# Optimization experiments

Measured on AMD Instinct MI355X. Metric: run time of the kernel, lower is better.

Reference implementation:

```python
import jax, jax.numpy as jnp
import numpy as np

EPS = 1e-5


def conv1x1(x, w, b):
    # x: [b,c,h,w], w: [o,c], b: [o] -> [b,o,h,w]  (1x1 conv == channel matmul)
    return jnp.einsum('bchw,oc->bohw', x, w) + b[None, :, None, None]


def nor_mean_std(x):
    # instance norm over spatial dims (torch calc_mean_std uses unbiased var)
    mean = jnp.mean(x, axis=(2, 3), keepdims=True)
    var = jnp.var(x, axis=(2, 3), keepdims=True, ddof=1)
    return (x - mean) / jnp.sqrt(var + EPS)


def nor_mean(x):
    mean = jnp.mean(x, axis=(2, 3), keepdims=True)
    return x - mean, mean


def net(x, w1, b1, w2, b2):
    return conv1x1(jax.nn.relu(conv1x1(x, w1, b1)), w2, b2)


def setup_inputs() -> dict:
    key = jax.random.key(0)
    ks = jax.random.split(key, 8)
    B, C, H, W = 8, 256, 128, 128
    return {
        'content': jax.random.normal(ks[0], (B, C, H, W), jnp.float32),
        'style': jax.random.normal(ks[1], (B, C, H, W), jnp.float32),
        'w1': jax.random.normal(ks[2], (128, 256), jnp.float32) * 0.05,
        'b1': jax.random.normal(ks[3], (128,), jnp.float32) * 0.05,
        'w2': jax.random.normal(ks[4], (32, 128), jnp.float32) * 0.05,
        'b2': jax.random.normal(ks[5], (32,), jnp.float32) * 0.05,
        'wu': jax.random.normal(ks[6], (256, 32), jnp.float32) * 0.05,
        'bu': jax.random.normal(ks[7], (256,), jnp.float32) * 0.05,
    }


def reference(content, style, w1, b1, w2, b2, wu, bu):
    cF_nor = nor_mean_std(content)
    sF_nor, smean = nor_mean(style)
    cF = net(cF_nor, w1, b1, w2, b2)          # [b,32,h,w]
    sF = net(sF_nor, w1, b1, w2, b2)          # [b,32,h,w]
    b, c, h, w = cF.shape
    hw = h * w
    sf = sF.reshape(b, c, hw)
    # channel covariance: [b,32,32]
    s_cov = jnp.einsum('bcn,bdn->bcd', sf, sf) / hw
    s_cov = jax.nn.softmax(s_cov, axis=-1) * (c ** -0.5)
    gF = jnp.einsum('bcd,bdn->bcn', s_cov, cF.reshape(b, c, hw)).reshape(b, c, h, w)
    gF = conv1x1(gF, wu, bu)                  # [b,256,h,w]
    return gF + smean + content
```

## Files before the change

### kernel.cpp

```cpp
#include <hip/hip_runtime.h>

#define HW 16384
#define C_IN 256
#define C_MID 128
#define C_OUT 32
#define EPSF 1e-5f

typedef __bf16 bf16x8 __attribute__((ext_vector_type(8)));
typedef __bf16 bf16x4 __attribute__((ext_vector_type(4)));
typedef float f32x4 __attribute__((ext_vector_type(4)));

__device__ __forceinline__ bf16x4 cvt4(f32x4 v) {
    bf16x4 r;
    r[0] = (__bf16)v[0]; r[1] = (__bf16)v[1];
    r[2] = (__bf16)v[2]; r[3] = (__bf16)v[3];
    return r;
}

__global__ __launch_bounds__(512) void k_stats10(const float* __restrict__ content,
                                                 const float* __restrict__ style,
                                                 float* __restrict__ cmean,
                                                 float* __restrict__ crstd,
                                                 float* __restrict__ smean,
                                                 __bf16* __restrict__ cbf,
                                                 __bf16* __restrict__ sbf) {
    const int bc = blockIdx.x;
    const int t = threadIdx.x;
    const f32x4* cp = (const f32x4*)(content + (size_t)bc * HW);
    const f32x4* sp = (const f32x4*)(style + (size_t)bc * HW);
    const int phase = (bc * 257) & 4095;

    int idx[8];
    #pragma unroll
    for (int i = 0; i < 8; ++i) idx[i] = (phase + t + i * 512) & 4095;

    f32x4 c[8], s[8];
    #pragma unroll
    for (int i = 0; i < 8; ++i) c[i] = __builtin_nontemporal_load(cp + idx[i]);
    #pragma unroll
    for (int i = 0; i < 8; ++i) s[i] = __builtin_nontemporal_load(sp + idx[i]);
    asm volatile("" ::
        "v"(c[0]), "v"(c[1]), "v"(c[2]), "v"(c[3]), "v"(c[4]), "v"(c[5]), "v"(c[6]), "v"(c[7]),
        "v"(s[0]), "v"(s[1]), "v"(s[2]), "v"(s[3]), "v"(s[4]), "v"(s[5]), "v"(s[6]), "v"(s[7]));

    {
        bf16x4* cb = (bf16x4*)(cbf + (size_t)bc * HW);
        bf16x4* sb = (bf16x4*)(sbf + (size_t)bc * HW);
        #pragma unroll
        for (int i = 0; i < 8; ++i) {
            cb[idx[i]] = cvt4(c[i]);
            sb[idx[i]] = cvt4(s[i]);
        }
    }

    float cs, cq, ss;
    {
        f32x4 a01 = c[0] + c[1], a23 = c[2] + c[3], a45 = c[4] + c[5], a67 = c[6] + c[7];
        f32x4 a = (a01 + a23) + (a45 + a67);
        cs = (a[0] + a[1]) + (a[2] + a[3]);
        f32x4 q01 = c[0]*c[0] + c[1]*c[1], q23 = c[2]*c[2] + c[3]*c[3];
        f32x4 q45 = c[4]*c[4] + c[5]*c[5], q67 = c[6]*c[6] + c[7]*c[7];
        f32x4 q = (q01 + q23) + (q45 + q67);
        cq = (q[0] + q[1]) + (q[2] + q[3]);
        f32x4 b01 = s[0] + s[1], b23 = s[2] + s[3], b45 = s[4] + s[5], b67 = s[6] + s[7];
        f32x4 bsum = (b01 + b23) + (b45 + b67);
        ss = (bsum[0] + bsum[1]) + (bsum[2] + bsum[3]);
    }

    #pragma unroll
    for (int d = 32; d > 0; d >>= 1) {
        cs += __shfl_xor(cs, d, 64);
        cq += __shfl_xor(cq, d, 64);
        ss += __shfl_xor(ss, d, 64);
    }
    __shared__ float rs[8], rq[8], rss[8];
    const int wv = t >> 6;
    if ((t & 63) == 0) { rs[wv] = cs; rq[wv] = cq; rss[wv] = ss; }
    __syncthreads();
    if (t == 0) {
        float S = 0.f, Q = 0.f, SS = 0.f;
        #pragma unroll
        for (int i = 0; i < 8; ++i) { S += rs[i]; Q += rq[i]; SS += rss[i]; }
        float n = (float)HW;
        float var = (Q - S * S / n) / (n - 1.f);
        cmean[bc] = S / n;
        crstd[bc] = 1.f / sqrtf(var + EPSF);
        smean[bc] = SS / n;
    }
}

__global__ __launch_bounds__(256) void k_wprep2(const float* __restrict__ w1,
                                                const float* __restrict__ b1,
                                                const float* __restrict__ w2,
                                                const float* __restrict__ cmean,
                                                const float* __restrict__ crstd,
                                                const float* __restrict__ smean,
                                                __bf16* __restrict__ W1c,
                                                float* __restrict__ bias1c,
                                                __bf16* __restrict__ W1s,
                                                float* __restrict__ bias1s,
                                                __bf16* __restrict__ W2b) {
    int o = blockIdx.x, b = blockIdx.y, t = threadIdx.x;
    float w = w1[o * 256 + t];
    float r = crstd[b * 256 + t];
    float wc = w * r;
    W1c[((size_t)(b * 128 + o)) * 256 + t] = (__bf16)wc;
    if (b == 0) {
        W1s[o * 256 + t] = (__bf16)w;
        if (t < 32) W2b[o * 32 + t] = (__bf16)w2[o * 32 + t];
    }
    float pc = wc * cmean[b * 256 + t];
    float ps = w * smean[b * 256 + t];
    __shared__ float rA[256], rB[256];
    rA[t] = pc; rB[t] = ps;
    __syncthreads();
    for (int off = 128; off > 0; off >>= 1) {
        if (t < off) { rA[t] += rA[t + off]; rB[t] += rB[t + off]; }
        __syncthreads();
    }
    if (t == 0) {
        bias1c[b * 128 + o] = b1[o] - rA[0];
        bias1s[b * 128 + o] = b1[o] - rB[0];
    }
}

template <int MODE>
__global__ __launch_bounds__(256) void k_net_bf(const __bf16* __restrict__ x,
                                                const __bf16* __restrict__ W1,
                                                const float* __restrict__ bias1,
                                                const __bf16* __restrict__ W2,
                                                const float* __restrict__ b2,
                                                float* __restrict__ outF,
                                                float* __restrict__ partial,
                                                int w1_per_batch) {
    __shared__ __bf16 Xl[64 * 256];
    __shared__ __bf16 Tl[64 * 128];
    const int tid = threadIdx.x;
    const int l = tid & 63, wv = tid >> 6;
    const int lr = l & 15, g = l >> 4;
    const int sw = (lr & 7) << 4;
    const int p0 = blockIdx.x * 64;
    const int b = blockIdx.y;
    const __bf16* xb = x + (size_t)b * C_IN * HW;

    {
        const int p = wv * 16 + lr;
        const __bf16* xp = xb + p0 + p;
        char* row = (char*)&Xl[p * 256];
        #pragma unroll 4
        for (int cc = 0; cc < 16; ++cc) {
            const int c = cc * 16 + g * 4;
            bf16x4 v;
            v[0] = xp[(size_t)(c + 0) * HW];
            v[1] = xp[(size_t)(c + 1) * HW];
            v[2] = xp[(size_t)(c + 2) * HW];
            v[3] = xp[(size_t)(c + 3) * HW];
            *(bf16x4*)(row + ((c * 2) ^ sw)) = v;
        }
    }
    __syncthreads();

    const f32x4 zero4 = {0.f, 0.f, 0.f, 0.f};
    f32x4 acc[2][4];
    #pragma unroll
    for (int mt = 0; mt < 2; ++mt)
        #pragma unroll
        for (int nt = 0; nt < 4; ++nt) acc[mt][nt] = zero4;

    const __bf16* W1b = W1 + (w1_per_batch ? ((size_t)b << 15) : 0);
    const __bf16* wrow0 = W1b + (size_t)(wv * 32 + lr) * 256 + g * 8;
    const __bf16* wrow1 = wrow0 + 16 * 256;

    #pragma unroll
    for (int kt = 0; kt < 8; ++kt) {
        bf16x8 a0 = *(const bf16x8*)(wrow0 + kt * 32);
        bf16x8 a1 = *(const bf16x8*)(wrow1 + kt * 32);
        #pragma unroll
        for (int nt = 0; nt < 4; ++nt) {
            const char* xrow = (const char*)&Xl[(nt * 16 + lr) * 256];
            bf16x8 bfr = *(const bf16x8*)(xrow + (((kt * 32 + g * 8) * 2) ^ sw));
            acc[0][nt] = __builtin_amdgcn_mfma_f32_16x16x32_bf16(a0, bfr, acc[0][nt], 0, 0, 0);
            acc[1][nt] = __builtin_amdgcn_mfma_f32_16x16x32_bf16(a1, bfr, acc[1][nt], 0, 0, 0);
        }
    }

    float4 bia[2];
    bia[0] = *(const float4*)&bias1[b * 128 + wv * 32 + g * 4];
    bia[1] = *(const float4*)&bias1[b * 128 + wv * 32 + 16 + g * 4];
    __syncthreads();
    #pragma unroll
    for (int mt = 0; mt < 2; ++mt) {
        #pragma unroll
        for (int nt = 0; nt < 4; ++nt) {
            const int p = nt * 16 + lr;
            char* trow = (char*)&Tl[p * 128];
            const int ob = (wv * 32 + mt * 16 + g * 4) * 2;
            bf16x4 tv;
            tv[0] = (__bf16)fmaxf(acc[mt][nt][0] + bia[mt].x, 0.f);
            tv[1] = (__bf16)fmaxf(acc[mt][nt][1] + bia[mt].y, 0.f);
            tv[2] = (__bf16)fmaxf(acc[mt][nt][2] + bia[mt].z, 0.f);
            tv[3] = (__bf16)fmaxf(acc[mt][nt][3] + bia[mt].w, 0.f);
            *(bf16x4*)(trow + (ob ^ sw)) = tv;
        }
    }
    __syncthreads();

    f32x4 acc2[2];
    acc2[0] = zero4; acc2[1] = zero4;
    const int p = wv * 16 + lr;
    const char* trow = (const char*)&Tl[p * 128];
    const __bf16* w2r0 = W2 + (size_t)lr * 128 + g * 8;
    const __bf16* w2r1 = w2r0 + 16 * 128;
    #pragma unroll
    for (int kt = 0; kt < 4; ++kt) {
        bf16x8 bfr = *(const bf16x8*)(trow + (((kt * 32 + g * 8) * 2) ^ sw));
        bf16x8 a0 = *(const bf16x8*)(w2r0 + kt * 32);
        bf16x8 a1 = *(const bf16x8*)(w2r1 + kt * 32);
        acc2[0] = __builtin_amdgcn_mfma_f32_16x16x32_bf16(a0, bfr, acc2[0], 0, 0, 0);
        acc2[1] = __builtin_amdgcn_mfma_f32_16x16x32_bf16(a1, bfr, acc2[1], 0, 0, 0);
    }
    float4 bb0 = *(const float4*)&b2[g * 4];
    float4 bb1 = *(const float4*)&b2[16 + g * 4];
    const int o0 = g * 4;

    if constexpr (MODE == 0) {
        float* ob = outF + (size_t)b * C_OUT * HW + p0 + p;
        ob[(size_t)(o0 + 0) * HW] = acc2[0][0] + bb0.x;
        ob[(size_t)(o0 + 1) * HW] = acc2[0][1] + bb0.y;
        ob[(size_t)(o0 + 2) * HW] = acc2[0][2] + bb0.z;
        ob[(size_t)(o0 + 3) * HW] = acc2[0][3] + bb0.w;
        ob[(size_t)(16 + o0 + 0) * HW] = acc2[1][0] + bb1.x;
        ob[(size_t)(16 + o0 + 1) * HW] = acc2[1][1] + bb1.y;
        ob[(size_t)(16 + o0 + 2) * HW] = acc2[1][2] + bb1.z;
        ob[(size_t)(16 + o0 + 3) * HW] = acc2[1][3] + bb1.w;
    } else {
        float* gt = (float*)Xl;
        gt[(o0 + 0) * 65 + p] = acc2[0][0] + bb0.x;
        gt[(o0 + 1) * 65 + p] = acc2[0][1] + bb0.y;
        gt[(o0 + 2) * 65 + p] = acc2[0][2] + bb0.z;
        gt[(o0 + 3) * 65 + p] = acc2[0][3] + bb0.w;
        gt[(16 + o0 + 0) * 65 + p] = acc2[1][0] + bb1.x;
        gt[(16 + o0 + 1) * 65 + p] = acc2[1][1] + bb1.y;
        gt[(16 + o0 + 2) * 65 + p] = acc2[1][2] + bb1.z;
        gt[(16 + o0 + 3) * 65 + p] = acc2[1][3] + bb1.w;
        __syncthreads();
        const int gi = tid >> 3, jb = (tid & 7) * 4;
        float g4[4] = {0.f, 0.f, 0.f, 0.f};
        #pragma unroll 8
        for (int n = 0; n < 64; ++n) {
            float si = gt[gi * 65 + n];
            #pragma unroll
            for (int q = 0; q < 4; ++q)
                g4[q] = fmaf(si, gt[(jb + q) * 65 + n], g4[q]);
        }
        float* dst = partial + ((size_t)(b * 256 + blockIdx.x)) * 1024 + tid * 4;
        #pragma unroll
        for (int q = 0; q < 4; ++q) dst[q] = g4[q];
    }
}

__global__ __launch_bounds__(1024) void k_softmax2(const float* __restrict__ partial,
                                                   float* __restrict__ scov) {
    int b = blockIdx.x;
    int j = threadIdx.x, i = threadIdx.y;
    const float* base = partial + (size_t)b * 256 * 1024 + i * 32 + j;
    float v0 = 0.f, v1 = 0.f, v2 = 0.f, v3 = 0.f;
    #pragma unroll 4
    for (int s = 0; s < 256; s += 4) {
        v0 += base[(s + 0) * 1024];
        v1 += base[(s + 1) * 1024];
        v2 += base[(s + 2) * 1024];
        v3 += base[(s + 3) * 1024];
    }
    float v = ((v0 + v1) + (v2 + v3)) * (1.f / (float)HW);
    float m = v;
    #pragma unroll
    for (int d = 16; d > 0; d >>= 1) m = fmaxf(m, __shfl_xor(m, d, 32));
    float e = expf(v - m);
    float sum = e;
    #pragma unroll
    for (int d = 16; d > 0; d >>= 1) sum += __shfl_xor(sum, d, 32);
    scov[(size_t)b * 1024 + i * 32 + j] = e / sum * 0.17677669529663687f;
}

__global__ __launch_bounds__(256) void k_final3(const float* __restrict__ cF,
                                                const float* __restrict__ scov,
                                                const float* __restrict__ wu,
                                                const float* __restrict__ bu,
                                                const float* __restrict__ smean,
                                                const __bf16* __restrict__ cbf,
                                                float* __restrict__ out) {
    __shared__ float sCov[1024];
    __shared__ float sC[32 * 64];
    __shared__ float sG[32 * 64];
    int t = threadIdx.x;
    int p0 = blockIdx.x * 64;
    int b = blockIdx.y;
    #pragma unroll
    for (int q = 0; q < 4; ++q) sCov[t + 256 * q] = scov[(size_t)b * 1024 + t + 256 * q];
    {
        int p = t & 63, rb = t >> 6;
        #pragma unroll
        for (int pass = 0; pass < 8; ++pass) {
            int r = pass * 4 + rb;
            sC[r * 64 + p] = cF[(size_t)b * C_OUT * HW + (size_t)r * HW + p0 + p];
        }
    }
    __syncthreads();
    {
        int gp = t & 63, gib = (t >> 6) * 8;
        #pragma unroll
        for (int rr = 0; rr < 8; ++rr) {
            int gi = gib + rr;
            float a = 0.f;
            #pragma unroll
            for (int k = 0; k < 32; ++k)
                a = fmaf(sCov[gi * 32 + k], sC[k * 64 + gp], a);
            sG[gi * 64 + gp] = a;
        }
    }
    __syncthreads();
    int tx = t & 7, ty = t >> 3;
    const float* wurow = wu + (size_t)(ty * 8) * 32;
    float acc[8][8];
    #pragma unroll
    for (int i = 0; i < 8; ++i)
        #pragma unroll
        for (int j = 0; j < 8; ++j) acc[i][j] = 0.f;
    #pragma unroll 4
    for (int k = 0; k < 32; ++k) {
        float a[8];
        #pragma unroll
        for (int i = 0; i < 8; ++i) a[i] = wurow[i * 32 + k];
        float4 b4a = *(const float4*)&sG[k * 64 + tx * 8];
        float4 b4b = *(const float4*)&sG[k * 64 + tx * 8 + 4];
        float bb[8] = {b4a.x, b4a.y, b4a.z, b4a.w, b4b.x, b4b.y, b4b.z, b4b.w};
        #pragma unroll
        for (int i = 0; i < 8; ++i)
            #pragma unroll
            for (int j = 0; j < 8; ++j)
                acc[i][j] = fmaf(a[i], bb[j], acc[i][j]);
    }
    #pragma unroll
    for (int i = 0; i < 8; ++i) {
        int o = ty * 8 + i;
        float add = bu[o] + smean[b * 256 + o];
        const __bf16* csrc = cbf + (size_t)b * C_IN * HW + (size_t)o * HW + p0 + tx * 8;
        float* dst = out + (size_t)b * C_IN * HW + (size_t)o * HW + p0 + tx * 8;
        bf16x8 cvv = *(const bf16x8*)csrc;
        f32x4 r0 = {acc[i][0] + add + (float)cvv[0], acc[i][1] + add + (float)cvv[1],
                    acc[i][2] + add + (float)cvv[2], acc[i][3] + add + (float)cvv[3]};
        f32x4 r1 = {acc[i][4] + add + (float)cvv[4], acc[i][5] + add + (float)cvv[5],
                    acc[i][6] + add + (float)cvv[6], acc[i][7] + add + (float)cvv[7]};
        __builtin_nontemporal_store(r0, (f32x4*)dst);
        __builtin_nontemporal_store(r1, (f32x4*)(dst + 4));
    }
}

extern "C" void kernel_launch(void* const* d_in, const int* in_sizes, int n_in,
                              void* d_out, int out_size, void* d_ws, size_t ws_size,
                              hipStream_t stream) {
    const float* content = (const float*)d_in[0];
    const float* style   = (const float*)d_in[1];
    const float* w1      = (const float*)d_in[2];
    const float* b1      = (const float*)d_in[3];
    const float* w2      = (const float*)d_in[4];
    const float* b2      = (const float*)d_in[5];
    const float* wu      = (const float*)d_in[6];
    const float* bu      = (const float*)d_in[7];
    float* out = (float*)d_out;
    float* ws  = (float*)d_ws;

    float* cmean   = ws;
    float* crstd   = ws + 2048;
    float* smean   = ws + 4096;
    float* scov    = ws + 6144;
    float* bias1c  = ws + 14336;
    float* bias1s  = ws + 15360;
    __bf16* W2b    = (__bf16*)(ws + 16384);
    __bf16* W1s    = (__bf16*)(ws + 18432);
    __bf16* W1c    = (__bf16*)(ws + 34816);
    float* partial = ws + 165888;
    float* cF      = ws + 2263040;
    __bf16* cbf    = (__bf16*)(ws + 6457344);
    __bf16* sbf    = (__bf16*)(ws + 23234560);

    k_stats10<<<dim3(2048), 512, 0, stream>>>(content, style, cmean, crstd, smean, cbf, sbf);
    k_wprep2<<<dim3(128, 8), 256, 0, stream>>>(w1, b1, w2, cmean, crstd, smean,
                                               W1c, bias1c, W1s, bias1s, W2b);
    k_net_bf<0><<<dim3(256, 8), 256, 0, stream>>>(cbf, W1c, bias1c, W2b, b2, cF, nullptr, 1);
    k_net_bf<1><<<dim3(256, 8), 256, 0, stream>>>(sbf, W1s, bias1s, W2b, b2, nullptr, partial, 0);
    k_softmax2<<<dim3(8), dim3(32, 32), 0, stream>>>(partial, scov);
    k_final3<<<dim3(256, 8), 256, 0, stream>>>(cF, scov, wu, bu, smean, cbf, out);
}
```

Measured before the change: 245.4 us.

## Fuse content net into final kernel, drop cF round trip and reuse staged content

Moves the content-branch net (two 1x1 convs on bf16 content) into the final kernel. cF is no longer written to and read back from global memory. The residual content values are now read from the bf16 tile already staged in shared memory instead of being loaded again from global. This removes one launch and the cF traffic, at the cost of more shared memory per block (the Xl, Tl, sCov and sG buffers together) and lower occupancy in the fused kernel.

```diff
diff --git a/kernel.cpp b/kernel.cpp
--- a/kernel.cpp
+++ b/kernel.cpp
@@ -124,15 +124,12 @@
     }
 }
 
-template <int MODE>
-__global__ __launch_bounds__(256) void k_net_bf(const __bf16* __restrict__ x,
-                                                const __bf16* __restrict__ W1,
-                                                const float* __restrict__ bias1,
-                                                const __bf16* __restrict__ W2,
-                                                const float* __restrict__ b2,
-                                                float* __restrict__ outF,
-                                                float* __restrict__ partial,
-                                                int w1_per_batch) {
+__global__ __launch_bounds__(256) void k_net_s(const __bf16* __restrict__ x,
+                                               const __bf16* __restrict__ W1,
+                                               const float* __restrict__ bias1,
+                                               const __bf16* __restrict__ W2,
+                                               const float* __restrict__ b2,
+                                               float* __restrict__ partial) {
     __shared__ __bf16 Xl[64 * 256];
     __shared__ __bf16 Tl[64 * 128];
     const int tid = threadIdx.x;
@@ -167,8 +164,7 @@
         #pragma unroll
         for (int nt = 0; nt < 4; ++nt) acc[mt][nt] = zero4;
 
-    const __bf16* W1b = W1 + (w1_per_batch ? ((size_t)b << 15) : 0);
-    const __bf16* wrow0 = W1b + (size_t)(wv * 32 + lr) * 256 + g * 8;
+    const __bf16* wrow0 = W1 + (size_t)(wv * 32 + lr) * 256 + g * 8;
     const __bf16* wrow1 = wrow0 + 16 * 256;
 
     #pragma unroll
@@ -223,40 +219,28 @@
     float4 bb1 = *(const float4*)&b2[16 + g * 4];
     const int o0 = g * 4;
 
-    if constexpr (MODE == 0) {
-        float* ob = outF + (size_t)b * C_OUT * HW + p0 + p;
-        ob[(size_t)(o0 + 0) * HW] = acc2[0][0] + bb0.x;
-        ob[(size_t)(o0 + 1) * HW] = acc2[0][1] + bb0.y;
-        ob[(size_t)(o0 + 2) * HW] = acc2[0][2] + bb0.z;
-        ob[(size_t)(o0 + 3) * HW] = acc2[0][3] + bb0.w;
-        ob[(size_t)(16 + o0 + 0) * HW] = acc2[1][0] + bb1.x;
-        ob[(size_t)(16 + o0 + 1) * HW] = acc2[1][1] + bb1.y;
-        ob[(size_t)(16 + o0 + 2) * HW] = acc2[1][2] + bb1.z;
-        ob[(size_t)(16 + o0 + 3) * HW] = acc2[1][3] + bb1.w;
-    } else {
-        float* gt = (float*)Xl;
-        gt[(o0 + 0) * 65 + p] = acc2[0][0] + bb0.x;
-        gt[(o0 + 1) * 65 + p] = acc2[0][1] + bb0.y;
-        gt[(o0 + 2) * 65 + p] = acc2[0][2] + bb0.z;
-        gt[(o0 + 3) * 65 + p] = acc2[0][3] + bb0.w;
-        gt[(16 + o0 + 0) * 65 + p] = acc2[1][0] + bb1.x;
-        gt[(16 + o0 + 1) * 65 + p] = acc2[1][1] + bb1.y;
-        gt[(16 + o0 + 2) * 65 + p] = acc2[1][2] + bb1.z;
-        gt[(16 + o0 + 3) * 65 + p] = acc2[1][3] + bb1.w;
-        __syncthreads();
-        const int gi = tid >> 3, jb = (tid & 7) * 4;
-        float g4[4] = {0.f, 0.f, 0.f, 0.f};
-        #pragma unroll 8
-        for (int n = 0; n < 64; ++n) {
-            float si = gt[gi * 65 + n];
-            #pragma unroll
-            for (int q = 0; q < 4; ++q)
-                g4[q] = fmaf(si, gt[(jb + q) * 65 + n], g4[q]);
-        }
-        float* dst = partial + ((size_t)(b * 256 + blockIdx.x)) * 1024 + tid * 4;
-        #pragma unroll
-        for (int q = 0; q < 4; ++q) dst[q] = g4[q];
-    }
+    float* gt = (float*)Xl;
+    gt[(o0 + 0) * 65 + p] = acc2[0][0] + bb0.x;
+    gt[(o0 + 1) * 65 + p] = acc2[0][1] + bb0.y;
+    gt[(o0 + 2) * 65 + p] = acc2[0][2] + bb0.z;
+    gt[(o0 + 3) * 65 + p] = acc2[0][3] + bb0.w;
+    gt[(16 + o0 + 0) * 65 + p] = acc2[1][0] + bb1.x;
+    gt[(16 + o0 + 1) * 65 + p] = acc2[1][1] + bb1.y;
+    gt[(16 + o0 + 2) * 65 + p] = acc2[1][2] + bb1.z;
+    gt[(16 + o0 + 3) * 65 + p] = acc2[1][3] + bb1.w;
+    __syncthreads();
+    const int gi = tid >> 3, jb = (tid & 7) * 4;
+    float g4[4] = {0.f, 0.f, 0.f, 0.f};
+    #pragma unroll 8
+    for (int n = 0; n < 64; ++n) {
+        float si = gt[gi * 65 + n];
+        #pragma unroll
+        for (int q = 0; q < 4; ++q)
+            g4[q] = fmaf(si, gt[(jb + q) * 65 + n], g4[q]);
+    }
+    float* dst = partial + ((size_t)(b * 256 + blockIdx.x)) * 1024 + tid * 4;
+    #pragma unroll
+    for (int q = 0; q < 4; ++q) dst[q] = g4[q];
 }
 
 __global__ __launch_bounds__(1024) void k_softmax2(const float* __restrict__ partial,
@@ -283,32 +267,126 @@
     scov[(size_t)b * 1024 + i * 32 + j] = e / sum * 0.17677669529663687f;
 }
 
-__global__ __launch_bounds__(256) void k_final3(const float* __restrict__ cF,
-                                                const float* __restrict__ scov,
-                                                const float* __restrict__ wu,
-                                                const float* __restrict__ bu,
-                                                const float* __restrict__ smean,
-                                                const __bf16* __restrict__ cbf,
-                                                float* __restrict__ out) {
+__global__ __launch_bounds__(256) void k_netc_final(const __bf16* __restrict__ x,
+                                                    const __bf16* __restrict__ W1,
+                                                    const float* __restrict__ bias1,
+                                                    const __bf16* __restrict__ W2,
+                                                    const float* __restrict__ b2,
+                                                    const float* __restrict__ scov,
+                                                    const float* __restrict__ wu,
+                                                    const float* __restrict__ bu,
+                                                    const float* __restrict__ smean,
+                                                    float* __restrict__ out) {
+    __shared__ __bf16 Xl[64 * 256];
+    __shared__ __bf16 Tl[64 * 128];
     __shared__ float sCov[1024];
-    __shared__ float sC[32 * 64];
     __shared__ float sG[32 * 64];
-    int t = threadIdx.x;
-    int p0 = blockIdx.x * 64;
-    int b = blockIdx.y;
-    #pragma unroll
-    for (int q = 0; q < 4; ++q) sCov[t + 256 * q] = scov[(size_t)b * 1024 + t + 256 * q];
-    {
-        int p = t & 63, rb = t >> 6;
-        #pragma unroll
-        for (int pass = 0; pass < 8; ++pass) {
-            int r = pass * 4 + rb;
-            sC[r * 64 + p] = cF[(size_t)b * C_OUT * HW + (size_t)r * HW + p0 + p];
-        }
-    }
-    __syncthreads();
-    {
-        int gp = t & 63, gib = (t >> 6) * 8;
+    const int tid = threadIdx.x;
+    const int l = tid & 63, wv = tid >> 6;
+    const int lr = l & 15, g = l >> 4;
+    const int sw = (lr & 7) << 4;
+    const int p0 = blockIdx.x * 64;
+    const int b = blockIdx.y;
+    const __bf16* xb = x + (size_t)b * C_IN * HW;
+
+    #pragma unroll
+    for (int q = 0; q < 4; ++q)
+        sCov[tid + 256 * q] = scov[(size_t)b * 1024 + tid + 256 * q];
+    {
+        const int p = wv * 16 + lr;
+        const __bf16* xp = xb + p0 + p;
+        char* row = (char*)&Xl[p * 256];
+        #pragma unroll 4
+        for (int cc = 0; cc < 16; ++cc) {
+            const int c = cc * 16 + g * 4;
+            bf16x4 v;
+            v[0] = xp[(size_t)(c + 0) * HW];
+            v[1] = xp[(size_t)(c + 1) * HW];
+            v[2] = xp[(size_t)(c + 2) * HW];
+            v[3] = xp[(size_t)(c + 3) * HW];
+            *(bf16x4*)(row + ((c * 2) ^ sw)) = v;
+        }
+    }
+    __syncthreads();
+
+    const f32x4 zero4 = {0.f, 0.f, 0.f, 0.f};
+    f32x4 acc1[2][4];
+    #pragma unroll
+    for (int mt = 0; mt < 2; ++mt)
+        #pragma unroll
+        for (int nt = 0; nt < 4; ++nt) acc1[mt][nt] = zero4;
+
+    const __bf16* W1b = W1 + ((size_t)b << 15);
+    const __bf16* wrow0 = W1b + (size_t)(wv * 32 + lr) * 256 + g * 8;
+    const __bf16* wrow1 = wrow0 + 16 * 256;
+
+    #pragma unroll
+    for (int kt = 0; kt < 8; ++kt) {
+        bf16x8 a0 = *(const bf16x8*)(wrow0 + kt * 32);
+        bf16x8 a1 = *(const bf16x8*)(wrow1 + kt * 32);
+        #pragma unroll
+        for (int nt = 0; nt < 4; ++nt) {
+            const char* xrow = (const char*)&Xl[(nt * 16 + lr) * 256];
+            bf16x8 bfr = *(const bf16x8*)(xrow + (((kt * 32 + g * 8) * 2) ^ sw));
+            acc1[0][nt] = __builtin_amdgcn_mfma_f32_16x16x32_bf16(a0, bfr, acc1[0][nt], 0, 0, 0);
+            acc1[1][nt] = __builtin_amdgcn_mfma_f32_16x16x32_bf16(a1, bfr, acc1[1][nt], 0, 0, 0);
+        }
+    }
+
+    float4 bia[2];
+    bia[0] = *(const float4*)&bias1[b * 128 + wv * 32 + g * 4];
+    bia[1] = *(const float4*)&bias1[b * 128 + wv * 32 + 16 + g * 4];
+    #pragma unroll
+    for (int mt = 0; mt < 2; ++mt) {
+        #pragma unroll
+        for (int nt = 0; nt < 4; ++nt) {
+            const int p = nt * 16 + lr;
+            char* trow = (char*)&Tl[p * 128];
+            const int ob = (wv * 32 + mt * 16 + g * 4) * 2;
+            bf16x4 tv;
+            tv[0] = (__bf16)fmaxf(acc1[mt][nt][0] + bia[mt].x, 0.f);
+            tv[1] = (__bf16)fmaxf(acc1[mt][nt][1] + bia[mt].y, 0.f);
+            tv[2] = (__bf16)fmaxf(acc1[mt][nt][2] + bia[mt].z, 0.f);
+            tv[3] = (__bf16)fmaxf(acc1[mt][nt][3] + bia[mt].w, 0.f);
+            *(bf16x4*)(trow + (ob ^ sw)) = tv;
+        }
+    }
+    __syncthreads();
+
+    f32x4 acc2[2];
+    acc2[0] = zero4; acc2[1] = zero4;
+    const int p = wv * 16 + lr;
+    {
+        const char* trow = (const char*)&Tl[p * 128];
+        const __bf16* w2r0 = W2 + (size_t)lr * 128 + g * 8;
+        const __bf16* w2r1 = w2r0 + 16 * 128;
+        #pragma unroll
+        for (int kt = 0; kt < 4; ++kt) {
+            bf16x8 bfr = *(const bf16x8*)(trow + (((kt * 32 + g * 8) * 2) ^ sw));
+            bf16x8 a0 = *(const bf16x8*)(w2r0 + kt * 32);
+            bf16x8 a1 = *(const bf16x8*)(w2r1 + kt * 32);
+            acc2[0] = __builtin_amdgcn_mfma_f32_16x16x32_bf16(a0, bfr, acc2[0], 0, 0, 0);
+            acc2[1] = __builtin_amdgcn_mfma_f32_16x16x32_bf16(a1, bfr, acc2[1], 0, 0, 0);
+        }
+    }
+    float4 bb0 = *(const float4*)&b2[g * 4];
+    float4 bb1 = *(const float4*)&b2[16 + g * 4];
+    const int o0 = g * 4;
+
+    __syncthreads();
+    float* sC = (float*)Tl;
+    sC[(o0 + 0) * 64 + p] = acc2[0][0] + bb0.x;
+    sC[(o0 + 1) * 64 + p] = acc2[0][1] + bb0.y;
+    sC[(o0 + 2) * 64 + p] = acc2[0][2] + bb0.z;
+    sC[(o0 + 3) * 64 + p] = acc2[0][3] + bb0.w;
+    sC[(16 + o0 + 0) * 64 + p] = acc2[1][0] + bb1.x;
+    sC[(16 + o0 + 1) * 64 + p] = acc2[1][1] + bb1.y;
+    sC[(16 + o0 + 2) * 64 + p] = acc2[1][2] + bb1.z;
+    sC[(16 + o0 + 3) * 64 + p] = acc2[1][3] + bb1.w;
+    __syncthreads();
+
+    {
+        int gp = tid & 63, gib = (tid >> 6) * 8;
         #pragma unroll
         for (int rr = 0; rr < 8; ++rr) {
             int gi = gib + rr;
@@ -320,7 +398,8 @@
         }
     }
     __syncthreads();
-    int tx = t & 7, ty = t >> 3;
+
+    const int tx = tid & 7, ty = tid >> 3;
     const float* wurow = wu + (size_t)(ty * 8) * 32;
     float acc[8][8];
     #pragma unroll
@@ -341,17 +420,23 @@
             for (int j = 0; j < 8; ++j)
                 acc[i][j] = fmaf(a[i], bb[j], acc[i][j]);
     }
+    float cvv[8][8];
+    #pragma unroll
+    for (int j = 0; j < 8; ++j) {
+        const int pl = tx * 8 + j;
+        bf16x8 rv = *(const bf16x8*)((const char*)Xl + pl * 512 + ((ty * 16) ^ (j << 4)));
+        #pragma unroll
+        for (int i = 0; i < 8; ++i) cvv[i][j] = (float)rv[i];
+    }
     #pragma unroll
     for (int i = 0; i < 8; ++i) {
         int o = ty * 8 + i;
         float add = bu[o] + smean[b * 256 + o];
-        const __bf16* csrc = cbf + (size_t)b * C_IN * HW + (size_t)o * HW + p0 + tx * 8;
         float* dst = out + (size_t)b * C_IN * HW + (size_t)o * HW + p0 + tx * 8;
-        bf16x8 cvv = *(const bf16x8*)csrc;
-        f32x4 r0 = {acc[i][0] + add + (float)cvv[0], acc[i][1] + add + (float)cvv[1],
-                    acc[i][2] + add + (float)cvv[2], acc[i][3] + add + (float)cvv[3]};
-        f32x4 r1 = {acc[i][4] + add + (float)cvv[4], acc[i][5] + add + (float)cvv[5],
-                    acc[i][6] + add + (float)cvv[6], acc[i][7] + add + (float)cvv[7]};
+        f32x4 r0 = {acc[i][0] + add + cvv[i][0], acc[i][1] + add + cvv[i][1],
+                    acc[i][2] + add + cvv[i][2], acc[i][3] + add + cvv[i][3]};
+        f32x4 r1 = {acc[i][4] + add + cvv[i][4], acc[i][5] + add + cvv[i][5],
+                    acc[i][6] + add + cvv[i][6], acc[i][7] + add + cvv[i][7]};
         __builtin_nontemporal_store(r0, (f32x4*)dst);
         __builtin_nontemporal_store(r1, (f32x4*)(dst + 4));
     }
@@ -381,15 +466,14 @@
     __bf16* W1s    = (__bf16*)(ws + 18432);
     __bf16* W1c    = (__bf16*)(ws + 34816);
     float* partial = ws + 165888;
-    float* cF      = ws + 2263040;
-    __bf16* cbf    = (__bf16*)(ws + 6457344);
-    __bf16* sbf    = (__bf16*)(ws + 23234560);
+    __bf16* cbf    = (__bf16*)(ws + 2263040);
+    __bf16* sbf    = (__bf16*)(ws + 19040256);
 
     k_stats10<<<dim3(2048), 512, 0, stream>>>(content, style, cmean, crstd, smean, cbf, sbf);
     k_wprep2<<<dim3(128, 8), 256, 0, stream>>>(w1, b1, w2, cmean, crstd, smean,
                                                W1c, bias1c, W1s, bias1s, W2b);
-    k_net_bf<0><<<dim3(256, 8), 256, 0, stream>>>(cbf, W1c, bias1c, W2b, b2, cF, nullptr, 1);
-    k_net_bf<1><<<dim3(256, 8), 256, 0, stream>>>(sbf, W1s, bias1s, W2b, b2, nullptr, partial, 0);
+    k_net_s<<<dim3(256, 8), 256, 0, stream>>>(sbf, W1s, bias1s, W2b, b2, partial);
     k_softmax2<<<dim3(8), dim3(32, 32), 0, stream>>>(partial, scov);
-    k_final3<<<dim3(256, 8), 256, 0, stream>>>(cF, scov, wu, bu, smean, cbf, out);
-}
+    k_netc_final<<<dim3(256, 8), 256, 0, stream>>>(cbf, W1c, bias1c, W2b, b2,
+                                                   scov, wu, bu, smean, out);
+}
```

New measurement: 223.0 us. 1.1x faster.
